# Performance work log

Measured on AMD Instinct MI355X. Metric: run time of the kernel, lower is better.

The kernel has to match this reference:

```python
import jax, jax.numpy as jnp
import numpy as np

B, N, E, H, D, F = 2, 4096, 128, 8, 16, 512
EPS = 1e-6


def _rms_norm(x, w):
    xf = x.astype(jnp.float32)
    n = xf * jax.lax.rsqrt(jnp.mean(xf * xf, axis=-1, keepdims=True) + EPS)
    return n.astype(x.dtype) * w


def setup_inputs() -> dict:
    key = jax.random.key(0)
    ks = jax.random.split(key, 12)
    s = 1.0 / np.sqrt(E)
    sf = 1.0 / np.sqrt(F)
    coords = jax.random.uniform(ks[10], (B, N, 2))
    dis = jnp.sqrt(jnp.sum((coords[:, :, None, :] - coords[:, None, :, :]) ** 2, -1))
    dis = dis * (1.0 - jnp.eye(N))  # zero diagonal
    return {
        "input1": jax.random.normal(ks[0], (B, N, E), jnp.float32),
        "dis_matrix": dis.astype(jnp.float32),
        "Wq": jax.random.uniform(ks[1], (E, E), jnp.float32, -s, s),
        "Wk": jax.random.uniform(ks[2], (E, E), jnp.float32, -s, s),
        "Wv": jax.random.uniform(ks[3], (E, E), jnp.float32, -s, s),
        "alpha": jnp.float32(1.0),
        "ln1_w": jnp.ones((E,), jnp.float32),
        "ln2_w": jnp.ones((E,), jnp.float32),
        "Wcomb": jax.random.uniform(ks[4], (E, E), jnp.float32, -s, s),
        "W1": jax.random.uniform(ks[5], (F, E), jnp.float32, -s, s),
        "b1": jax.random.uniform(ks[6], (F,), jnp.float32, -s, s),
        "W2": jax.random.uniform(ks[7], (E, F), jnp.float32, -sf, sf),
        "b2": jax.random.uniform(ks[8], (E,), jnp.float32, -sf, sf),
    }


def _sparse_attention_afm(x, dis_matrix, Wq, Wk, Wv, alpha):
    # project and split heads: [B,N,E] -> [B,H,N,D]
    def heads(w):
        return (x @ w.T).reshape(B, N, H, D).transpose(0, 2, 1, 3)
    q, k, v = heads(Wq), heads(Wk), heads(Wv)
    log2n = jnp.float32(np.log2(N))
    dis_weight = jnp.exp(-alpha * log2n * dis_matrix)  # [B,N,N] (i,j)
    k_weight = jnp.exp(k)  # [B,H,N,D]
    w1 = jnp.einsum('bij,bhik->bhjk', dis_weight, k_weight * v)
    w2 = jnp.einsum('bij,bhik->bhjk', dis_weight, k_weight)
    out = jax.nn.sigmoid(q) * (w1 / w2)  # [B,H,N,D]
    return out.transpose(0, 2, 1, 3).reshape(B, N, E)


def reference(input1, dis_matrix, Wq, Wk, Wv, alpha, ln1_w, ln2_w, Wcomb, W1, b1, W2, b2):
    h = _rms_norm(input1, ln1_w)
    attn = _sparse_attention_afm(h, dis_matrix, Wq, Wk, Wv, alpha)
    out1 = input1 + attn @ Wcomb.T
    h2 = _rms_norm(out1, ln2_w)
    ffn = jax.nn.relu(h2 @ W1.T + b1) @ W2.T + b2
    return out1 + ffn
```

## Files before the change

### kernel.cpp

```cpp
#include <hip/hip_runtime.h>

#define NTOK 4096
#define EDIM 128

typedef __attribute__((ext_vector_type(8))) short bf16x8;
typedef __attribute__((ext_vector_type(4))) float f32x4;

__device__ __forceinline__ ushort f2bf(float x) {
    union { float f; unsigned u; } c; c.f = x;
    unsigned r = c.u + 0x7FFF + ((c.u >> 16) & 1);
    return (ushort)(r >> 16);
}

__device__ __forceinline__ void stage_w(const float* __restrict__ W, ushort* Bs) {
    const int t = threadIdx.x;
    const int br = t >> 1, h = (t & 1) * 64;
    const float* src = W + (size_t)br * 128 + h;
    ushort* dst = Bs + br * 136 + h;
#pragma unroll
    for (int j = 0; j < 8; ++j) {
        float4 u = *(const float4*)(src + j * 8);
        float4 v = *(const float4*)(src + j * 8 + 4);
        bf16x8 o;
        o[0] = (short)f2bf(u.x); o[1] = (short)f2bf(u.y);
        o[2] = (short)f2bf(u.z); o[3] = (short)f2bf(u.w);
        o[4] = (short)f2bf(v.x); o[5] = (short)f2bf(v.y);
        o[6] = (short)f2bf(v.z); o[7] = (short)f2bf(v.w);
        *(bf16x8*)(dst + j * 8) = o;
    }
}

__device__ __forceinline__ void gemm128(const ushort* __restrict__ As,
                                        const ushort* __restrict__ Bs,
                                        f32x4 (&acc)[2][2], int lane, int wv) {
    const int m15 = lane & 15, kq = (lane >> 4) * 8, c0w = wv * 32;
#pragma unroll
    for (int kc = 0; kc < 4; ++kc) {
        int ko = kc * 32 + kq;
        bf16x8 a0 = *(const bf16x8*)&As[m15 * 136 + ko];
        bf16x8 a1 = *(const bf16x8*)&As[(16 + m15) * 136 + ko];
        bf16x8 b0 = *(const bf16x8*)&Bs[(c0w + m15) * 136 + ko];
        bf16x8 b1 = *(const bf16x8*)&Bs[(c0w + 16 + m15) * 136 + ko];
        acc[0][0] = __builtin_amdgcn_mfma_f32_16x16x32_bf16(a0, b0, acc[0][0], 0, 0, 0);
        acc[0][1] = __builtin_amdgcn_mfma_f32_16x16x32_bf16(a0, b1, acc[0][1], 0, 0, 0);
        acc[1][0] = __builtin_amdgcn_mfma_f32_16x16x32_bf16(a1, b0, acc[1][0], 0, 0, 0);
        acc[1][1] = __builtin_amdgcn_mfma_f32_16x16x32_bf16(a1, b1, acc[1][1], 0, 0, 0);
    }
}

__launch_bounds__(256, 2)
__global__ void qkv_k(const float* __restrict__ input1, const float* __restrict__ ln1w,
                      const float* __restrict__ Wq, const float* __restrict__ Wk,
                      const float* __restrict__ Wv,
                      const float* __restrict__ Wc, const float* __restrict__ W1,
                      const float* __restrict__ W2, ushort* __restrict__ Wbf,
                      float* __restrict__ sigq, ushort* __restrict__ Mt) {
    const int bx = blockIdx.x;
    if (bx >= 256) {
        int g = ((bx - 256) * 256 + threadIdx.x) * 4;
        const float* src; ushort* dst;
        if (g < 16384)      { src = Wc + g;           dst = Wbf + 49152 + g; }
        else if (g < 81920) { src = W1 + (g - 16384); dst = Wbf + 65536 + (g - 16384); }
        else                { src = W2 + (g - 81920); dst = Wbf + 131072 + (g - 81920); }
        float4 u = *(const float4*)src;
        ushort4 o; o.x = f2bf(u.x); o.y = f2bf(u.y); o.z = f2bf(u.z); o.w = f2bf(u.w);
        *(ushort4*)dst = o;
        return;
    }
    __shared__ ushort As[32 * 136];
    __shared__ ushort Bs0[128 * 136];
    __shared__ ushort Bs1[128 * 136];
    const int t = threadIdx.x, lane = t & 63, wv = t >> 6;
    const int m15 = lane & 15, quad = lane >> 4, c0w = wv * 32;
    const int M0 = bx * 32;

    {
        const int row = t >> 3, seg = t & 7;
        const float* xp = input1 + (size_t)(M0 + row) * 128 + seg * 16;
        float4 x[4]; float ss = 0.f;
#pragma unroll
        for (int i = 0; i < 4; ++i) {
            x[i] = *(const float4*)(xp + i * 4);
            ss += x[i].x * x[i].x + x[i].y * x[i].y + x[i].z * x[i].z + x[i].w * x[i].w;
        }
        ss += __shfl_down(ss, 4, 8);
        ss += __shfl_down(ss, 2, 8);
        ss += __shfl_down(ss, 1, 8);
        ss = __shfl(ss, 0, 8);
        float rr = rsqrtf(ss * (1.0f / 128.0f) + 1e-6f);
#pragma unroll
        for (int i = 0; i < 4; ++i) {
            float4 w4 = *(const float4*)&ln1w[seg * 16 + i * 4];
            ushort4 o;
            o.x = f2bf(x[i].x * rr * w4.x);
            o.y = f2bf(x[i].y * rr * w4.y);
            o.z = f2bf(x[i].z * rr * w4.z);
            o.w = f2bf(x[i].w * rr * w4.w);
            *(ushort4*)&As[row * 136 + seg * 16 + i * 4] = o;
        }
    }
    stage_w(Wq, Bs0);
    __syncthreads();
    {
        f32x4 acc[2][2] = {};
        gemm128(As, Bs0, acc, lane, wv);
        stage_w(Wk, Bs1);
#pragma unroll
        for (int mi = 0; mi < 2; ++mi)
#pragma unroll
            for (int ni = 0; ni < 2; ++ni)
#pragma unroll
                for (int r = 0; r < 4; ++r) {
                    int row = M0 + mi * 16 + quad * 4 + r;
                    int lc  = c0w + ni * 16 + m15;
                    sigq[(size_t)row * 128 + lc] = 1.0f / (1.0f + __expf(-acc[mi][ni][r]));
                }
    }
    __syncthreads();
    f32x4 acck[2][2] = {};
    gemm128(As, Bs1, acck, lane, wv);
    stage_w(Wv, Bs0);
    __syncthreads();
    f32x4 accv[2][2] = {};
    gemm128(As, Bs0, accv, lane, wv);
    const int b = M0 >> 12, i0 = M0 & (NTOK - 1);
#pragma unroll
    for (int mi = 0; mi < 2; ++mi)
#pragma unroll
        for (int ni = 0; ni < 2; ++ni) {
            int e = c0w + ni * 16 + m15;
            ushort* mt0 = Mt + ((size_t)b * 256 + e) * NTOK;
            ushort* mt1 = mt0 + (size_t)128 * NTOK;
            int ib = i0 + mi * 16 + quad * 4;
            ushort4 pv, pk;
            float kw0 = __expf(acck[mi][ni][0]); pv.x = f2bf(kw0 * accv[mi][ni][0]); pk.x = f2bf(kw0);
            float kw1 = __expf(acck[mi][ni][1]); pv.y = f2bf(kw1 * accv[mi][ni][1]); pk.y = f2bf(kw1);
            float kw2 = __expf(acck[mi][ni][2]); pv.z = f2bf(kw2 * accv[mi][ni][2]); pk.z = f2bf(kw2);
            float kw3 = __expf(acck[mi][ni][3]); pv.w = f2bf(kw3 * accv[mi][ni][3]); pk.w = f2bf(kw3);
            *(ushort4*)&mt0[ib] = pv;
            *(ushort4*)&mt1[ib] = pk;
        }
}

__launch_bounds__(512, 2)
__global__ void big_gemm_k(const float* __restrict__ dis, const float* __restrict__ alphap,
                           const ushort* __restrict__ Mt,
                           float* __restrict__ P0, float* __restrict__ P1) {
    __shared__ ushort As[64 * 72];
    const int P = blockIdx.x;
    const int q = (P & 7) >> 1;
    const int b = q & 1, s = q >> 1;
    const int j0 = (((P >> 3) << 1) | (P & 1)) * 64;
    const int t = threadIdx.x, lane = t & 63, wv = t >> 6;
    const int m15 = lane & 15, quad = lane >> 4, kq = quad * 8;
    const float coef = -alphap[0] * 12.0f;
    const float* disb = dis + (size_t)b * NTOK * NTOK;
    const ushort* Mtb = Mt + (size_t)b * 256 * NTOK;
    float* outp = ((s == 0) ? P0 : P1) + (size_t)b * NTOK * 256;
    const int k0 = s * (NTOK / 2);

    const int aj = t >> 3, ak = (t & 7) * 8;
    const float* arow = disb + (size_t)(j0 + aj) * NTOK;
    const int c0 = wv * 32;
    const ushort* Bp = Mtb + (size_t)(c0 + m15) * NTOK + kq;

    f32x4 acc[4][2] = {};
    float4 fA0, fA1, fB0, fB1;
    bf16x8 pb[2][2], pbn[2][2];
    fA0 = *(const float4*)(arow + k0 + ak);
    fA1 = *(const float4*)(arow + k0 + ak + 4);
    fB0 = *(const float4*)(arow + k0 + 64 + ak);
    fB1 = *(const float4*)(arow + k0 + 64 + ak + 4);
#pragma unroll
    for (int kh = 0; kh < 2; ++kh)
#pragma unroll
        for (int ni = 0; ni < 2; ++ni)
            pb[kh][ni] = *(const bf16x8*)&Bp[(size_t)(ni * 16) * NTOK + k0 + kh * 32];

#define BIG_ITER(FA0, FA1, PBC, PBN, IT) do {                                   \
    bf16x8 a8;                                                                  \
    a8[0] = (short)f2bf(__expf(coef * FA0.x));                                  \
    a8[1] = (short)f2bf(__expf(coef * FA0.y));                                  \
    a8[2] = (short)f2bf(__expf(coef * FA0.z));                                  \
    a8[3] = (short)f2bf(__expf(coef * FA0.w));                                  \
    a8[4] = (short)f2bf(__expf(coef * FA1.x));                                  \
    a8[5] = (short)f2bf(__expf(coef * FA1.y));                                  \
    a8[6] = (short)f2bf(__expf(coef * FA1.z));                                  \
    a8[7] = (short)f2bf(__expf(coef * FA1.w));                                  \
    *(bf16x8*)&As[aj * 72 + ak] = a8;                                           \
    __syncthreads();                                                            \
    {   int itA = (IT) + 2; int ka = (itA < 32) ? k0 + itA * 64 : k0;           \
        FA0 = *(const float4*)(arow + ka + ak);                                 \
        FA1 = *(const float4*)(arow + ka + ak + 4);                             \
        int itB = (IT) + 1; int kb_ = (itB < 32) ? k0 + itB * 64 : k0;          \
        _Pragma("unroll") for (int kh = 0; kh < 2; ++kh)                        \
        _Pragma("unroll") for (int ni = 0; ni < 2; ++ni)                        \
            PBN[kh][ni] = *(const bf16x8*)&Bp[(size_t)(ni * 16) * NTOK + kb_ + kh * 32]; } \
    _Pragma("unroll") for (int kh = 0; kh < 2; ++kh) {                          \
        bf16x8 av0 = *(const bf16x8*)&As[(m15) * 72 + kh * 32 + kq];            \
        bf16x8 av1 = *(const bf16x8*)&As[(16 + m15) * 72 + kh * 32 + kq];       \
        bf16x8 av2 = *(const bf16x8*)&As[(32 + m15) * 72 + kh * 32 + kq];       \
        bf16x8 av3 = *(const bf16x8*)&As[(48 + m15) * 72 + kh * 32 + kq];       \
        acc[0][0] = __builtin_amdgcn_mfma_f32_16x16x32_bf16(av0, PBC[kh][0], acc[0][0], 0, 0, 0); \
        acc[0][1] = __builtin_amdgcn_mfma_f32_16x16x32_bf16(av0, PBC[kh][1], acc[0][1], 0, 0, 0); \
        acc[1][0] = __builtin_amdgcn_mfma_f32_16x16x32_bf16(av1, PBC[kh][0], acc[1][0], 0, 0, 0); \
        acc[1][1] = __builtin_amdgcn_mfma_f32_16x16x32_bf16(av1, PBC[kh][1], acc[1][1], 0, 0, 0); \
        acc[2][0] = __builtin_amdgcn_mfma_f32_16x16x32_bf16(av2, PBC[kh][0], acc[2][0], 0, 0, 0); \
        acc[2][1] = __builtin_amdgcn_mfma_f32_16x16x32_bf16(av2, PBC[kh][1], acc[2][1], 0, 0, 0); \
        acc[3][0] = __builtin_amdgcn_mfma_f32_16x16x32_bf16(av3, PBC[kh][0], acc[3][0], 0, 0, 0); \
        acc[3][1] = __builtin_amdgcn_mfma_f32_16x16x32_bf16(av3, PBC[kh][1], acc[3][1], 0, 0, 0); \
    }                                                                           \
    __syncthreads();                                                            \
} while (0)

    for (int it2 = 0; it2 < 16; ++it2) {
        BIG_ITER(fA0, fA1, pb, pbn, it2 * 2);
        BIG_ITER(fB0, fB1, pbn, pb, it2 * 2 + 1);
    }
#undef BIG_ITER

#pragma unroll
    for (int mi = 0; mi < 4; ++mi)
#pragma unroll
        for (int ni = 0; ni < 2; ++ni)
#pragma unroll
            for (int r = 0; r < 4; ++r) {
                int j = j0 + mi * 16 + quad * 4 + r;
                int c = c0 + ni * 16 + m15;
                outp[(size_t)j * 256 + c] = acc[mi][ni][r];
            }
}

__launch_bounds__(256, 1)
__global__ void tail_k(const float* __restrict__ sigq,
                       const float* __restrict__ P0, const float* __restrict__ P1,
                       const ushort* __restrict__ Wbf,
                       const float* __restrict__ input1, const float* __restrict__ b1,
                       const float* __restrict__ b2, const float* __restrict__ ln2w,
                       float* __restrict__ out) {
    __shared__ ushort As[32 * 136];
    __shared__ ushort As2[32 * 136];
    __shared__ ushort Bs[128 * 136];
    __shared__ ushort Bs2[128 * 136];
    __shared__ float  O[32][132];
    const int t = threadIdx.x, lane = t & 63, wv = t >> 6;
    const int m15 = lane & 15, quad = lane >> 4, c0w = wv * 32;
    const int M0 = blockIdx.x * 32;

    {
        const int ar = t >> 3, e0 = (t & 7) * 16;
        const int g = M0 + ar;
        const float4* sg  = (const float4*)(sigq + (size_t)g * 128 + e0);
        const float4* p0a = (const float4*)(P0 + (size_t)g * 256 + e0);
        const float4* p1a = (const float4*)(P1 + (size_t)g * 256 + e0);
        const float4* p0b = (const float4*)(P0 + (size_t)g * 256 + 128 + e0);
        const float4* p1b = (const float4*)(P1 + (size_t)g * 256 + 128 + e0);
#pragma unroll
        for (int i = 0; i < 4; ++i) {
            float4 s = sg[i];
            float4 u0 = p0a[i], u1 = p1a[i], d0 = p0b[i], d1 = p1b[i];
            ushort4 a;
            a.x = f2bf(s.x * (u0.x + u1.x) / (d0.x + d1.x));
            a.y = f2bf(s.y * (u0.y + u1.y) / (d0.y + d1.y));
            a.z = f2bf(s.z * (u0.z + u1.z) / (d0.z + d1.z));
            a.w = f2bf(s.w * (u0.w + u1.w) / (d0.w + d1.w));
            *(ushort4*)&As[ar * 136 + e0 + i * 4] = a;
        }
    }
    {
        const int br = t >> 1, bs0 = (t & 1) * 8;
        const ushort* W = Wbf + 49152;
#pragma unroll
        for (int j = 0; j < 8; ++j) {
            int seg = bs0 + j;
            *(bf16x8*)&Bs[br * 136 + seg * 8] = *(const bf16x8*)&W[(size_t)br * 128 + seg * 8];
        }
    }
    __syncthreads();
    f32x4 acc[2][2] = {};
    gemm128(As, Bs, acc, lane, wv);
#pragma unroll
    for (int mi = 0; mi < 2; ++mi)
#pragma unroll
        for (int ni = 0; ni < 2; ++ni)
#pragma unroll
            for (int r = 0; r < 4; ++r) {
                int rl  = mi * 16 + quad * 4 + r;
                int col = c0w + ni * 16 + m15;
                O[rl][col] = acc[mi][ni][r] + input1[(size_t)(M0 + rl) * 128 + col];
            }
    __syncthreads();
    {
        const int row = t >> 3, seg = t & 7;
        float4 x[4]; float ss = 0.f;
#pragma unroll
        for (int i = 0; i < 4; ++i) {
            x[i] = *(const float4*)&O[row][seg * 16 + i * 4];
            ss += x[i].x * x[i].x + x[i].y * x[i].y + x[i].z * x[i].z + x[i].w * x[i].w;
        }
        ss += __shfl_down(ss, 4, 8);
        ss += __shfl_down(ss, 2, 8);
        ss += __shfl_down(ss, 1, 8);
        ss = __shfl(ss, 0, 8);
        float rr = rsqrtf(ss * (1.0f / 128.0f) + 1e-6f);
#pragma unroll
        for (int i = 0; i < 4; ++i) {
            float4 w4 = *(const float4*)&ln2w[seg * 16 + i * 4];
            ushort4 o;
            o.x = f2bf(x[i].x * rr * w4.x);
            o.y = f2bf(x[i].y * rr * w4.y);
            o.z = f2bf(x[i].z * rr * w4.z);
            o.w = f2bf(x[i].w * rr * w4.w);
            *(ushort4*)&As[row * 136 + seg * 16 + i * 4] = o;
        }
    }
    f32x4 aout[2][2] = {};
    for (int f0 = 0; f0 < 4; ++f0) {
        __syncthreads();
        {
            const int br = t >> 1, h = (t & 1) * 64;
            const ushort* w1 = Wbf + 65536 + (size_t)(f0 * 128 + br) * 128 + h;
            const ushort* w2 = Wbf + 131072 + (size_t)br * 512 + f0 * 128 + h;
            ushort* d1 = Bs + br * 136 + h;
            ushort* d2 = Bs2 + br * 136 + h;
#pragma unroll
            for (int j = 0; j < 8; ++j) {
                *(bf16x8*)(d1 + j * 8) = *(const bf16x8*)(w1 + j * 8);
                *(bf16x8*)(d2 + j * 8) = *(const bf16x8*)(w2 + j * 8);
            }
        }
        __syncthreads();
        f32x4 am[2][2] = {};
        gemm128(As, Bs, am, lane, wv);
#pragma unroll
        for (int mi = 0; mi < 2; ++mi)
#pragma unroll
            for (int ni = 0; ni < 2; ++ni)
#pragma unroll
                for (int r = 0; r < 4; ++r) {
                    int rl  = mi * 16 + quad * 4 + r;
                    int col = c0w + ni * 16 + m15;
                    As2[rl * 136 + col] = f2bf(fmaxf(am[mi][ni][r] + b1[f0 * 128 + col], 0.0f));
                }
        __syncthreads();
        gemm128(As2, Bs2, aout, lane, wv);
    }
#pragma unroll
    for (int mi = 0; mi < 2; ++mi)
#pragma unroll
        for (int ni = 0; ni < 2; ++ni)
#pragma unroll
            for (int r = 0; r < 4; ++r) {
                int rl  = mi * 16 + quad * 4 + r;
                int col = c0w + ni * 16 + m15;
                out[(size_t)(M0 + rl) * 128 + col] = (O[rl][col] + b2[col]) + aout[mi][ni][r];
            }
}

extern "C" void kernel_launch(void* const* d_in, const int* in_sizes, int n_in,
                              void* d_out, int out_size, void* d_ws, size_t ws_size,
                              hipStream_t stream) {
    const float* input1 = (const float*)d_in[0];
    const float* dis    = (const float*)d_in[1];
    const float* Wq     = (const float*)d_in[2];
    const float* Wk     = (const float*)d_in[3];
    const float* Wv     = (const float*)d_in[4];
    const float* alpha  = (const float*)d_in[5];
    const float* ln1    = (const float*)d_in[6];
    const float* ln2    = (const float*)d_in[7];
    const float* Wcomb  = (const float*)d_in[8];
    const float* W1     = (const float*)d_in[9];
    const float* b1     = (const float*)d_in[10];
    const float* W2     = (const float*)d_in[11];
    const float* b2     = (const float*)d_in[12];
    float* out = (float*)d_out;

    char* w8 = (char*)d_ws;
    ushort* Wbf  = (ushort*)(w8);
    float*  sigq = (float*)(w8 + (4u << 20));
    ushort* Mt   = (ushort*)(w8 + (8u << 20));
    float*  P0   = (float*)(w8 + (12u << 20));
    float*  P1   = (float*)(w8 + (20u << 20));

    qkv_k<<<dim3(400), 256, 0, stream>>>(input1, ln1, Wq, Wk, Wv,
                                         Wcomb, W1, W2, Wbf, sigq, Mt);
    big_gemm_k<<<dim3(256), 512, 0, stream>>>(dis, alpha, Mt, P0, P1);
    tail_k<<<dim3(256), 256, 0, stream>>>(sigq, P0, P1, Wbf, input1, b1, b2,
                                          ln2, out);
}
```

Measured before the change: 264.9 us.

## Drop split-K in big GEMM, use 32-row tiles and swizzled LDS, read weights directly

The big distance GEMM no longer splits K into two halves written to P0/P1. Each block now covers 32 rows over the full K range with an XOR-swizzled unpadded LDS tile, which removes the partial-sum writes and their reads in the tail kernel. The tail kernel also stops staging weight matrices in LDS and feeds B operands straight from global memory, with swizzled A tiles in LDS. The trade-off is that each block now runs twice as many K iterations with half the MFMA work per sync, and B fragments are read from global rather than from shared memory.

```diff
diff --git a/kernel.cpp b/kernel.cpp
--- a/kernel.cpp
+++ b/kernel.cpp
@@ -11,6 +11,9 @@
     unsigned r = c.u + 0x7FFF + ((c.u >> 16) & 1);
     return (ushort)(r >> 16);
 }
+
+__device__ __forceinline__ int swz64(int r, int k)  { return r * 64  + (k ^ ((r & 7) << 3)); }
+__device__ __forceinline__ int swz128(int r, int k) { return r * 128 + (k ^ ((r & 7) << 3)); }
 
 __device__ __forceinline__ void stage_w(const float* __restrict__ W, ushort* Bs) {
     const int t = threadIdx.x;
@@ -41,6 +44,24 @@
         bf16x8 a1 = *(const bf16x8*)&As[(16 + m15) * 136 + ko];
         bf16x8 b0 = *(const bf16x8*)&Bs[(c0w + m15) * 136 + ko];
         bf16x8 b1 = *(const bf16x8*)&Bs[(c0w + 16 + m15) * 136 + ko];
+        acc[0][0] = __builtin_amdgcn_mfma_f32_16x16x32_bf16(a0, b0, acc[0][0], 0, 0, 0);
+        acc[0][1] = __builtin_amdgcn_mfma_f32_16x16x32_bf16(a0, b1, acc[0][1], 0, 0, 0);
+        acc[1][0] = __builtin_amdgcn_mfma_f32_16x16x32_bf16(a1, b0, acc[1][0], 0, 0, 0);
+        acc[1][1] = __builtin_amdgcn_mfma_f32_16x16x32_bf16(a1, b1, acc[1][1], 0, 0, 0);
+    }
+}
+
+__device__ __forceinline__ void gemm_dirB(const ushort* __restrict__ As,
+                                          const ushort* __restrict__ W, int ldb,
+                                          f32x4 (&acc)[2][2], int lane, int wv) {
+    const int m15 = lane & 15, kq = (lane >> 4) * 8, c0w = wv * 32;
+#pragma unroll
+    for (int kc = 0; kc < 4; ++kc) {
+        int ko = kc * 32 + kq;
+        bf16x8 a0 = *(const bf16x8*)&As[swz128(m15, ko)];
+        bf16x8 a1 = *(const bf16x8*)&As[swz128(16 + m15, ko)];
+        bf16x8 b0 = *(const bf16x8*)&W[(size_t)(c0w + m15) * ldb + ko];
+        bf16x8 b1 = *(const bf16x8*)&W[(size_t)(c0w + 16 + m15) * ldb + ko];
         acc[0][0] = __builtin_amdgcn_mfma_f32_16x16x32_bf16(a0, b0, acc[0][0], 0, 0, 0);
         acc[0][1] = __builtin_amdgcn_mfma_f32_16x16x32_bf16(a0, b1, acc[0][1], 0, 0, 0);
         acc[1][0] = __builtin_amdgcn_mfma_f32_16x16x32_bf16(a1, b0, acc[1][0], 0, 0, 0);
@@ -144,83 +165,64 @@
 
 __launch_bounds__(512, 2)
 __global__ void big_gemm_k(const float* __restrict__ dis, const float* __restrict__ alphap,
-                           const ushort* __restrict__ Mt,
-                           float* __restrict__ P0, float* __restrict__ P1) {
-    __shared__ ushort As[64 * 72];
-    const int P = blockIdx.x;
-    const int q = (P & 7) >> 1;
-    const int b = q & 1, s = q >> 1;
-    const int j0 = (((P >> 3) << 1) | (P & 1)) * 64;
+                           const ushort* __restrict__ Mt, float* __restrict__ P) {
+    __shared__ ushort As[32 * 64];
     const int t = threadIdx.x, lane = t & 63, wv = t >> 6;
     const int m15 = lane & 15, quad = lane >> 4, kq = quad * 8;
+    const int b  = blockIdx.x & 1;
+    const int j0 = (blockIdx.x >> 1) * 32;
     const float coef = -alphap[0] * 12.0f;
-    const float* disb = dis + (size_t)b * NTOK * NTOK;
     const ushort* Mtb = Mt + (size_t)b * 256 * NTOK;
-    float* outp = ((s == 0) ? P0 : P1) + (size_t)b * NTOK * 256;
-    const int k0 = s * (NTOK / 2);
-
-    const int aj = t >> 3, ak = (t & 7) * 8;
-    const float* arow = disb + (size_t)(j0 + aj) * NTOK;
+    float* outp = P + (size_t)b * NTOK * 256;
+
+    const int sr = t >> 4, sk = (t & 15) * 4;
+    const float* arow = dis + (size_t)b * NTOK * NTOK + (size_t)(j0 + sr) * NTOK + sk;
     const int c0 = wv * 32;
-    const ushort* Bp = Mtb + (size_t)(c0 + m15) * NTOK + kq;
-
-    f32x4 acc[4][2] = {};
-    float4 fA0, fA1, fB0, fB1;
+
+    f32x4 acc[2][2] = {};
+    float4 fa_e, fa_o;
     bf16x8 pb[2][2], pbn[2][2];
-    fA0 = *(const float4*)(arow + k0 + ak);
-    fA1 = *(const float4*)(arow + k0 + ak + 4);
-    fB0 = *(const float4*)(arow + k0 + 64 + ak);
-    fB1 = *(const float4*)(arow + k0 + 64 + ak + 4);
+    fa_e = *(const float4*)(arow);
+    fa_o = *(const float4*)(arow + 64);
 #pragma unroll
     for (int kh = 0; kh < 2; ++kh)
 #pragma unroll
         for (int ni = 0; ni < 2; ++ni)
-            pb[kh][ni] = *(const bf16x8*)&Bp[(size_t)(ni * 16) * NTOK + k0 + kh * 32];
-
-#define BIG_ITER(FA0, FA1, PBC, PBN, IT) do {                                   \
-    bf16x8 a8;                                                                  \
-    a8[0] = (short)f2bf(__expf(coef * FA0.x));                                  \
-    a8[1] = (short)f2bf(__expf(coef * FA0.y));                                  \
-    a8[2] = (short)f2bf(__expf(coef * FA0.z));                                  \
-    a8[3] = (short)f2bf(__expf(coef * FA0.w));                                  \
-    a8[4] = (short)f2bf(__expf(coef * FA1.x));                                  \
-    a8[5] = (short)f2bf(__expf(coef * FA1.y));                                  \
-    a8[6] = (short)f2bf(__expf(coef * FA1.z));                                  \
-    a8[7] = (short)f2bf(__expf(coef * FA1.w));                                  \
-    *(bf16x8*)&As[aj * 72 + ak] = a8;                                           \
+            pb[kh][ni] = *(const bf16x8*)&Mtb[(size_t)(c0 + ni * 16 + m15) * NTOK + kh * 32 + kq];
+
+#define BIG_ITER(FA, PBC, PBN, IT) do {                                         \
+    ushort4 a4;                                                                 \
+    a4.x = f2bf(__expf(coef * FA.x));                                           \
+    a4.y = f2bf(__expf(coef * FA.y));                                           \
+    a4.z = f2bf(__expf(coef * FA.z));                                           \
+    a4.w = f2bf(__expf(coef * FA.w));                                           \
+    *(ushort4*)&As[swz64(sr, sk)] = a4;                                         \
     __syncthreads();                                                            \
-    {   int itA = (IT) + 2; int ka = (itA < 32) ? k0 + itA * 64 : k0;           \
-        FA0 = *(const float4*)(arow + ka + ak);                                 \
-        FA1 = *(const float4*)(arow + ka + ak + 4);                             \
-        int itB = (IT) + 1; int kb_ = (itB < 32) ? k0 + itB * 64 : k0;          \
+    {   int itA = (IT) + 2;                                                     \
+        if (itA < 64) FA = *(const float4*)(arow + itA * 64);                   \
+        int itB = (IT) + 1; int kb_ = (itB < 64) ? itB * 64 : 0;                \
         _Pragma("unroll") for (int kh = 0; kh < 2; ++kh)                        \
         _Pragma("unroll") for (int ni = 0; ni < 2; ++ni)                        \
-            PBN[kh][ni] = *(const bf16x8*)&Bp[(size_t)(ni * 16) * NTOK + kb_ + kh * 32]; } \
+            PBN[kh][ni] = *(const bf16x8*)&Mtb[(size_t)(c0 + ni * 16 + m15) * NTOK + kb_ + kh * 32 + kq]; } \
     _Pragma("unroll") for (int kh = 0; kh < 2; ++kh) {                          \
-        bf16x8 av0 = *(const bf16x8*)&As[(m15) * 72 + kh * 32 + kq];            \
-        bf16x8 av1 = *(const bf16x8*)&As[(16 + m15) * 72 + kh * 32 + kq];       \
-        bf16x8 av2 = *(const bf16x8*)&As[(32 + m15) * 72 + kh * 32 + kq];       \
-        bf16x8 av3 = *(const bf16x8*)&As[(48 + m15) * 72 + kh * 32 + kq];       \
-        acc[0][0] = __builtin_amdgcn_mfma_f32_16x16x32_bf16(av0, PBC[kh][0], acc[0][0], 0, 0, 0); \
-        acc[0][1] = __builtin_amdgcn_mfma_f32_16x16x32_bf16(av0, PBC[kh][1], acc[0][1], 0, 0, 0); \
-        acc[1][0] = __builtin_amdgcn_mfma_f32_16x16x32_bf16(av1, PBC[kh][0], acc[1][0], 0, 0, 0); \
-        acc[1][1] = __builtin_amdgcn_mfma_f32_16x16x32_bf16(av1, PBC[kh][1], acc[1][1], 0, 0, 0); \
-        acc[2][0] = __builtin_amdgcn_mfma_f32_16x16x32_bf16(av2, PBC[kh][0], acc[2][0], 0, 0, 0); \
-        acc[2][1] = __builtin_amdgcn_mfma_f32_16x16x32_bf16(av2, PBC[kh][1], acc[2][1], 0, 0, 0); \
-        acc[3][0] = __builtin_amdgcn_mfma_f32_16x16x32_bf16(av3, PBC[kh][0], acc[3][0], 0, 0, 0); \
-        acc[3][1] = __builtin_amdgcn_mfma_f32_16x16x32_bf16(av3, PBC[kh][1], acc[3][1], 0, 0, 0); \
+        bf16x8 a0 = *(const bf16x8*)&As[swz64(m15, kh * 32 + kq)];              \
+        bf16x8 a1 = *(const bf16x8*)&As[swz64(16 + m15, kh * 32 + kq)];         \
+        acc[0][0] = __builtin_amdgcn_mfma_f32_16x16x32_bf16(a0, PBC[kh][0], acc[0][0], 0, 0, 0); \
+        acc[0][1] = __builtin_amdgcn_mfma_f32_16x16x32_bf16(a0, PBC[kh][1], acc[0][1], 0, 0, 0); \
+        acc[1][0] = __builtin_amdgcn_mfma_f32_16x16x32_bf16(a1, PBC[kh][0], acc[1][0], 0, 0, 0); \
+        acc[1][1] = __builtin_amdgcn_mfma_f32_16x16x32_bf16(a1, PBC[kh][1], acc[1][1], 0, 0, 0); \
     }                                                                           \
     __syncthreads();                                                            \
 } while (0)
 
-    for (int it2 = 0; it2 < 16; ++it2) {
-        BIG_ITER(fA0, fA1, pb, pbn, it2 * 2);
-        BIG_ITER(fB0, fB1, pbn, pb, it2 * 2 + 1);
+    for (int it2 = 0; it2 < 32; ++it2) {
+        BIG_ITER(fa_e, pb, pbn, it2 * 2);
+        BIG_ITER(fa_o, pbn, pb, it2 * 2 + 1);
     }
 #undef BIG_ITER
 
 #pragma unroll
-    for (int mi = 0; mi < 4; ++mi)
+    for (int mi = 0; mi < 2; ++mi)
 #pragma unroll
         for (int ni = 0; ni < 2; ++ni)
 #pragma unroll
@@ -232,16 +234,13 @@
 }
 
 __launch_bounds__(256, 1)
-__global__ void tail_k(const float* __restrict__ sigq,
-                       const float* __restrict__ P0, const float* __restrict__ P1,
+__global__ void tail_k(const float* __restrict__ sigq, const float* __restrict__ P,
                        const ushort* __restrict__ Wbf,
                        const float* __restrict__ input1, const float* __restrict__ b1,
                        const float* __restrict__ b2, const float* __restrict__ ln2w,
                        float* __restrict__ out) {
-    __shared__ ushort As[32 * 136];
-    __shared__ ushort As2[32 * 136];
-    __shared__ ushort Bs[128 * 136];
-    __shared__ ushort Bs2[128 * 136];
+    __shared__ ushort As[32 * 128];
+    __shared__ ushort As2[32 * 128];
     __shared__ float  O[32][132];
     const int t = threadIdx.x, lane = t & 63, wv = t >> 6;
     const int m15 = lane & 15, quad = lane >> 4, c0w = wv * 32;
@@ -250,35 +249,23 @@
     {
         const int ar = t >> 3, e0 = (t & 7) * 16;
         const int g = M0 + ar;
-        const float4* sg  = (const float4*)(sigq + (size_t)g * 128 + e0);
-        const float4* p0a = (const float4*)(P0 + (size_t)g * 256 + e0);
-        const float4* p1a = (const float4*)(P1 + (size_t)g * 256 + e0);
-        const float4* p0b = (const float4*)(P0 + (size_t)g * 256 + 128 + e0);
-        const float4* p1b = (const float4*)(P1 + (size_t)g * 256 + 128 + e0);
-#pragma unroll
-        for (int i = 0; i < 4; ++i) {
-            float4 s = sg[i];
-            float4 u0 = p0a[i], u1 = p1a[i], d0 = p0b[i], d1 = p1b[i];
+        const float4* sg = (const float4*)(sigq + (size_t)g * 128 + e0);
+        const float4* pu = (const float4*)(P + (size_t)g * 256 + e0);
+        const float4* pd = (const float4*)(P + (size_t)g * 256 + 128 + e0);
+#pragma unroll
+        for (int i = 0; i < 4; ++i) {
+            float4 s = sg[i], u = pu[i], d = pd[i];
             ushort4 a;
-            a.x = f2bf(s.x * (u0.x + u1.x) / (d0.x + d1.x));
-            a.y = f2bf(s.y * (u0.y + u1.y) / (d0.y + d1.y));
-            a.z = f2bf(s.z * (u0.z + u1.z) / (d0.z + d1.z));
-            a.w = f2bf(s.w * (u0.w + u1.w) / (d0.w + d1.w));
-            *(ushort4*)&As[ar * 136 + e0 + i * 4] = a;
-        }
-    }
-    {
-        const int br = t >> 1, bs0 = (t & 1) * 8;
-        const ushort* W = Wbf + 49152;
-#pragma unroll
-        for (int j = 0; j < 8; ++j) {
-            int seg = bs0 + j;
-            *(bf16x8*)&Bs[br * 136 + seg * 8] = *(const bf16x8*)&W[(size_t)br * 128 + seg * 8];
+            a.x = f2bf(s.x * u.x / d.x);
+            a.y = f2bf(s.y * u.y / d.y);
+            a.z = f2bf(s.z * u.z / d.z);
+            a.w = f2bf(s.w * u.w / d.w);
+            *(ushort4*)&As[swz128(ar, e0 + i * 4)] = a;
         }
     }
     __syncthreads();
     f32x4 acc[2][2] = {};
-    gemm128(As, Bs, acc, lane, wv);
+    gemm_dirB(As, Wbf + 49152, 128, acc, lane, wv);
 #pragma unroll
     for (int mi = 0; mi < 2; ++mi)
 #pragma unroll
@@ -311,27 +298,14 @@
             o.y = f2bf(x[i].y * rr * w4.y);
             o.z = f2bf(x[i].z * rr * w4.z);
             o.w = f2bf(x[i].w * rr * w4.w);
-            *(ushort4*)&As[row * 136 + seg * 16 + i * 4] = o;
+            *(ushort4*)&As[swz128(row, seg * 16 + i * 4)] = o;
         }
     }
     f32x4 aout[2][2] = {};
     for (int f0 = 0; f0 < 4; ++f0) {
         __syncthreads();
-        {
-            const int br = t >> 1, h = (t & 1) * 64;
-            const ushort* w1 = Wbf + 65536 + (size_t)(f0 * 128 + br) * 128 + h;
-            const ushort* w2 = Wbf + 131072 + (size_t)br * 512 + f0 * 128 + h;
-            ushort* d1 = Bs + br * 136 + h;
-            ushort* d2 = Bs2 + br * 136 + h;
-#pragma unroll
-            for (int j = 0; j < 8; ++j) {
-                *(bf16x8*)(d1 + j * 8) = *(const bf16x8*)(w1 + j * 8);
-                *(bf16x8*)(d2 + j * 8) = *(const bf16x8*)(w2 + j * 8);
-            }
-        }
-        __syncthreads();
         f32x4 am[2][2] = {};
-        gemm128(As, Bs, am, lane, wv);
+        gemm_dirB(As, Wbf + 65536 + f0 * 128 * 128, 128, am, lane, wv);
 #pragma unroll
         for (int mi = 0; mi < 2; ++mi)
 #pragma unroll
@@ -340,10 +314,10 @@
                 for (int r = 0; r < 4; ++r) {
                     int rl  = mi * 16 + quad * 4 + r;
                     int col = c0w + ni * 16 + m15;
-                    As2[rl * 136 + col] = f2bf(fmaxf(am[mi][ni][r] + b1[f0 * 128 + col], 0.0f));
+                    As2[swz128(rl, col)] = f2bf(fmaxf(am[mi][ni][r] + b1[f0 * 128 + col], 0.0f));
                 }
         __syncthreads();
-        gemm128(As2, Bs2, aout, lane, wv);
+        gemm_dirB(As2, Wbf + 131072 + f0 * 128, 512, aout, lane, wv);
     }
 #pragma unroll
     for (int mi = 0; mi < 2; ++mi)
@@ -379,12 +353,10 @@
     ushort* Wbf  = (ushort*)(w8);
     float*  sigq = (float*)(w8 + (4u << 20));
     ushort* Mt   = (ushort*)(w8 + (8u << 20));
-    float*  P0   = (float*)(w8 + (12u << 20));
-    float*  P1   = (float*)(w8 + (20u << 20));
+    float*  P    = (float*)(w8 + (12u << 20));
 
     qkv_k<<<dim3(400), 256, 0, stream>>>(input1, ln1, Wq, Wk, Wv,
                                          Wcomb, W1, W2, Wbf, sigq, Mt);
-    big_gemm_k<<<dim3(256), 512, 0, stream>>>(dis, alpha, Mt, P0, P1);
-    tail_k<<<dim3(256), 256, 0, stream>>>(sigq, P0, P1, Wbf, input1, b1, b2,
-                                          ln2, out);
-}
+    big_gemm_k<<<dim3(256), 512, 0, stream>>>(dis, alpha, Mt, P);
+    tail_k<<<dim3(256), 256, 0, stream>>>(sigq, P, Wbf, input1, b1, b2, ln2, out);
+}
```

Result: slower. 286.7 us (+8.2%).
